# Optimization experiments

Measured on AMD Instinct MI355X. Metric: run time of the kernel, lower is better.

Reference implementation:

```python
import jax, jax.numpy as jnp
import numpy as np

B, S, DIM = 2, 2048, 2048
H, KVH, D = 16, 8, 128
EPS = 1e-6
ROPE_BASE = 1000000.0
MAX_SEQ = 8192


def _build_rope(max_seq, dim, base):
    inv_freq = 1.0 / (base ** (np.arange(0, dim, 2, dtype=np.float64) / dim))
    t = np.arange(max_seq, dtype=np.float64)
    freqs = np.outer(t, inv_freq)  # [max_seq, dim//2]
    return (jnp.asarray(np.cos(freqs), jnp.float32),
            jnp.asarray(np.sin(freqs), jnp.float32))


def setup_inputs() -> dict:
    key = jax.random.key(0)
    ks = jax.random.split(key, 7)
    scale = 0.02
    cos_cache, sin_cache = _build_rope(MAX_SEQ, D, ROPE_BASE)
    return {
        "x": jax.random.normal(ks[0], (B, S, DIM), jnp.float32),
        "wq": jax.random.normal(ks[1], (DIM, H * D), jnp.float32) * scale,
        "wk": jax.random.normal(ks[2], (DIM, KVH * D), jnp.float32) * scale,
        "wv": jax.random.normal(ks[3], (DIM, KVH * D), jnp.float32) * scale,
        "wo": jax.random.normal(ks[4], (H * D, DIM), jnp.float32) * scale,
        "q_gamma": 1.0 + 0.01 * jax.random.normal(ks[5], (D,), jnp.float32),
        "k_gamma": 1.0 + 0.01 * jax.random.normal(ks[6], (D,), jnp.float32),
        "cos_cache": cos_cache,
        "sin_cache": sin_cache,
    }


def _rmsnorm(t, gamma):
    var = jnp.mean(t * t, axis=-1, keepdims=True)
    return t * jax.lax.rsqrt(var + EPS) * gamma


def _rotate_half(t):
    t1, t2 = jnp.split(t, 2, axis=-1)
    return jnp.concatenate((-t2, t1), axis=-1)


def _apply_rope(t, cos, sin):
    # t: [B, S, heads, D]; cos/sin: [S, D//2]
    cos_f = jnp.concatenate((cos, cos), axis=-1)[None, :, None, :]
    sin_f = jnp.concatenate((sin, sin), axis=-1)[None, :, None, :]
    return t * cos_f + _rotate_half(t) * sin_f


def reference(x, wq, wk, wv, wo, q_gamma, k_gamma, cos_cache, sin_cache):
    b, s, _ = x.shape
    q = (x @ wq).reshape(b, s, H, D)
    k = (x @ wk).reshape(b, s, KVH, D)
    v = (x @ wv).reshape(b, s, KVH, D)
    q = _rmsnorm(q, q_gamma)
    k = _rmsnorm(k, k_gamma)
    # prefill: kv_len == q_len == s, cache empty
    cos, sin = cos_cache[:s], sin_cache[:s]
    q = _apply_rope(q, cos, sin)
    k = _apply_rope(k, cos, sin)
    # -> [B, heads, S, D]
    q = q.transpose(0, 2, 1, 3)
    k = k.transpose(0, 2, 1, 3)
    v = v.transpose(0, 2, 1, 3)
    # GQA: repeat_interleave kv heads
    g = H // KVH
    k = jnp.repeat(k, g, axis=1)
    v = jnp.repeat(v, g, axis=1)
    scale = 1.0 / jnp.sqrt(jnp.asarray(D, x.dtype))
    scores = jnp.einsum("bhqd,bhkd->bhqk", q, k) * scale
    causal = jnp.tril(jnp.ones((s, s), bool))
    scores = jnp.where(causal, scores, jnp.finfo(scores.dtype).min)
    attn = jax.nn.softmax(scores, axis=-1)
    out = jnp.einsum("bhqk,bhkd->bhqd", attn, v)
    out = out.transpose(0, 2, 1, 3).reshape(b, s, H * D)
    return out @ wo
```

## Files before the change

kernel.cpp:

```cpp
#include <hip/hip_runtime.h>
#include <hip/hip_bf16.h>


typedef __attribute__((ext_vector_type(8))) short s16x8;
typedef __attribute__((ext_vector_type(4))) float f32x4;

typedef const __attribute__((address_space(1))) void* gas_t;
typedef __attribute__((address_space(3))) void* las_t;
#define GLL16(g, l) __builtin_amdgcn_global_load_lds((gas_t)(const void*)(g), (las_t)(void*)(l), 16, 0, 0)

static __device__ __forceinline__ unsigned short f2bf(float f) {
    union { float f; unsigned u; } v; v.f = f;
    unsigned r = v.u + 0x7FFF + ((v.u >> 16) & 1);
    return (unsigned short)(r >> 16);
}
static __device__ __forceinline__ float bf2f(unsigned short h) {
    union { unsigned u; float f; } v; v.u = ((unsigned)h) << 16;
    return v.f;
}
static __device__ __forceinline__ float exp2_fast(float x) {
    float r; asm("v_exp_f32 %0, %1" : "=v"(r) : "v"(x)); return r;
}

#define SCALE_L2E 0.12751744900929f

__global__ __launch_bounds__(256) void k_convert_x(const float* __restrict__ x,
                                                   unsigned short* __restrict__ xb, int n) {
    int i = (blockIdx.x * 256 + threadIdx.x) * 8;
    if (i >= n) return;
    float4 a = *(const float4*)(x + i);
    float4 b = *(const float4*)(x + i + 4);
    s16x8 o;
    o[0] = (short)f2bf(a.x); o[1] = (short)f2bf(a.y); o[2] = (short)f2bf(a.z); o[3] = (short)f2bf(a.w);
    o[4] = (short)f2bf(b.x); o[5] = (short)f2bf(b.y); o[6] = (short)f2bf(b.z); o[7] = (short)f2bf(b.w);
    *(s16x8*)(xb + i) = o;
}

__global__ __launch_bounds__(256) void k_transpose_w(const float* __restrict__ src,
                                                     unsigned short* __restrict__ dst,
                                                     int K, int N, int nbase, int dstld) {
    __shared__ float t[32][33];
    int k0 = blockIdx.x * 32, n0 = blockIdx.y * 32;
    int tx = threadIdx.x & 31, ty0 = threadIdx.x >> 5;
    for (int p = 0; p < 4; p++) {
        int ty = ty0 + p * 8;
        t[ty][tx] = src[(size_t)(k0 + ty) * N + n0 + tx];
    }
    __syncthreads();
    for (int p = 0; p < 4; p++) {
        int ty = ty0 + p * 8;
        dst[(size_t)(nbase + n0 + ty) * dstld + k0 + tx] = f2bf(t[tx][ty]);
    }
}

__global__ __launch_bounds__(256) void k_transpose_v(const unsigned short* __restrict__ V,
                                                     unsigned short* __restrict__ Vt) {
    __shared__ unsigned short t[32][33];
    int s0 = blockIdx.x * 32, d0 = blockIdx.y * 32;
    size_t base = (size_t)blockIdx.z * 2048 * 128;
    int tx = threadIdx.x & 31, ty0 = threadIdx.x >> 5;
    for (int p = 0; p < 4; p++) {
        int ty = ty0 + p * 8;
        t[ty][tx] = V[base + (size_t)(s0 + ty) * 128 + d0 + tx];
    }
    __syncthreads();
    for (int p = 0; p < 4; p++) {
        int ty = ty0 + p * 8;
        Vt[base + (size_t)(d0 + ty) * 2048 + s0 + tx] = t[tx][ty];
    }
}

template<int OUTF32>
__global__ __launch_bounds__(512, 2) void k_gemm256(const unsigned short* __restrict__ A,
                                                    const unsigned short* __restrict__ Bt,
                                                    void* __restrict__ Cout,
                                                    int M, int N, int K) {
    __shared__ unsigned short Ls[2][2][2][8192];
    int tid = threadIdx.x, lane = tid & 63, wave = tid >> 6;
    int wm = wave >> 2, wn = wave & 3;
    int lr = lane & 15, lg = lane >> 4;
    int swrow = wave * 16 + (lane >> 2);
    int scol  = (lane & 3) * 8;
    const unsigned short* Ab = A  + (size_t)(blockIdx.x * 256) * K;
    const unsigned short* Bb = Bt + (size_t)(blockIdx.y * 256) * K;

    f32x4 acc[8][4] = {};
    int NK = K / 64;

    auto issue = [&](int slot, int mat, int kk, int k0) {
        const unsigned short* base = mat ? Bb : Ab;
        unsigned short* dst = &Ls[slot][mat][kk][wave * 512];
        GLL16(base + (size_t)swrow * K + k0 + kk * 32 + scol, dst);
        GLL16(base + (size_t)(swrow + 128) * K + k0 + kk * 32 + scol, dst + 4096);
    };

    issue(0, 0, 0, 0);
    issue(0, 1, 0, 0);
    issue(0, 0, 1, 0);
    issue(0, 1, 1, 0);

    for (int t = 0; t < NK; ++t) {
        int slot = t & 1, nslot = slot ^ 1;
        int kn = (t + 1) * 64;
        bool more = (t + 1) < NK;
        const unsigned short* As0 = Ls[slot][0][0];
        const unsigned short* Bs0 = Ls[slot][1][0];
        const unsigned short* As1 = Ls[slot][0][1];
        const unsigned short* Bs1 = Ls[slot][1][1];
        s16x8 af[4], bfr[4];

        asm volatile("s_waitcnt vmcnt(4)" ::: "memory");
        __builtin_amdgcn_s_barrier();
        asm volatile("" ::: "memory");

        #pragma unroll
        for (int m = 0; m < 4; m++) af[m]  = *(const s16x8*)&As0[(wm * 128 + m * 16 + lr) * 32 + lg * 8];
        #pragma unroll
        for (int n = 0; n < 4; n++) bfr[n] = *(const s16x8*)&Bs0[(wn * 64 + n * 16 + lr) * 32 + lg * 8];
        if (more) issue(nslot, 0, 0, kn);
        __builtin_amdgcn_s_setprio(1);
        #pragma unroll
        for (int m = 0; m < 4; m++)
            #pragma unroll
            for (int n = 0; n < 4; n++)
                acc[m][n] = __builtin_amdgcn_mfma_f32_16x16x32_bf16(af[m], bfr[n], acc[m][n], 0, 0, 0);
        __builtin_amdgcn_s_setprio(0);

        #pragma unroll
        for (int m = 0; m < 4; m++) af[m] = *(const s16x8*)&As0[(wm * 128 + (m + 4) * 16 + lr) * 32 + lg * 8];
        if (more) issue(nslot, 1, 0, kn);
        __builtin_amdgcn_s_setprio(1);
        #pragma unroll
        for (int m = 0; m < 4; m++)
            #pragma unroll
            for (int n = 0; n < 4; n++)
                acc[m + 4][n] = __builtin_amdgcn_mfma_f32_16x16x32_bf16(af[m], bfr[n], acc[m + 4][n], 0, 0, 0);
        __builtin_amdgcn_s_setprio(0);

        if (more) asm volatile("s_waitcnt vmcnt(4)" ::: "memory");
        else      asm volatile("s_waitcnt vmcnt(0)" ::: "memory");
        __builtin_amdgcn_s_barrier();
        asm volatile("" ::: "memory");

        #pragma unroll
        for (int m = 0; m < 4; m++) af[m]  = *(const s16x8*)&As1[(wm * 128 + m * 16 + lr) * 32 + lg * 8];
        #pragma unroll
        for (int n = 0; n < 4; n++) bfr[n] = *(const s16x8*)&Bs1[(wn * 64 + n * 16 + lr) * 32 + lg * 8];
        if (more) issue(nslot, 0, 1, kn);
        __builtin_amdgcn_s_setprio(1);
        #pragma unroll
        for (int m = 0; m < 4; m++)
            #pragma unroll
            for (int n = 0; n < 4; n++)
                acc[m][n] = __builtin_amdgcn_mfma_f32_16x16x32_bf16(af[m], bfr[n], acc[m][n], 0, 0, 0);
        __builtin_amdgcn_s_setprio(0);

        #pragma unroll
        for (int m = 0; m < 4; m++) af[m] = *(const s16x8*)&As1[(wm * 128 + (m + 4) * 16 + lr) * 32 + lg * 8];
        if (more) issue(nslot, 1, 1, kn);
        __builtin_amdgcn_s_setprio(1);
        #pragma unroll
        for (int m = 0; m < 4; m++)
            #pragma unroll
            for (int n = 0; n < 4; n++)
                acc[m + 4][n] = __builtin_amdgcn_mfma_f32_16x16x32_bf16(af[m], bfr[n], acc[m + 4][n], 0, 0, 0);
        __builtin_amdgcn_s_setprio(0);
    }

    int rbase = blockIdx.x * 256 + wm * 128;
    int cbase = blockIdx.y * 256 + wn * 64;
    #pragma unroll
    for (int am = 0; am < 8; am++)
        #pragma unroll
        for (int n = 0; n < 4; n++)
            #pragma unroll
            for (int r = 0; r < 4; r++) {
                int row = rbase + am * 16 + lg * 4 + r;
                int col = cbase + n * 16 + lr;
                float v = acc[am][n][r];
                if (OUTF32) ((float*)Cout)[(size_t)row * N + col] = v;
                else        ((unsigned short*)Cout)[(size_t)row * N + col] = f2bf(v);
            }
}

template<int OUTF32>
__global__ __launch_bounds__(256) void k_gemm_bt(const unsigned short* __restrict__ A,
                                                 const unsigned short* __restrict__ Bt,
                                                 void* __restrict__ Cout,
                                                 int M, int N, int K) {
    __shared__ unsigned short As[128 * 32];
    __shared__ unsigned short Bs[128 * 32];
    int tid = threadIdx.x;
    int lane = tid & 63;
    int wave = tid >> 6;
    int wm = wave >> 1, wn = wave & 1;
    int lr = lane & 15, lk = (lane >> 4) * 8;
    int srow = wave * 32 + (lane >> 2);
    int scol = (lane & 3) * 8;
    const unsigned short* Ag0 = A  + (size_t)(blockIdx.x * 128 + srow) * K + scol;
    const unsigned short* Ag1 = Ag0 + (size_t)16 * K;
    const unsigned short* Bg0 = Bt + (size_t)(blockIdx.y * 128 + srow) * K + scol;
    const unsigned short* Bg1 = Bg0 + (size_t)16 * K;
    unsigned short* Asw = &As[wave * 1024];
    unsigned short* Bsw = &Bs[wave * 1024];
    f32x4 acc[4][4] = {};
    for (int k0 = 0; k0 < K; k0 += 32) {
        __syncthreads();
        GLL16(Ag0 + k0, Asw);
        GLL16(Ag1 + k0, Asw + 512);
        GLL16(Bg0 + k0, Bsw);
        GLL16(Bg1 + k0, Bsw + 512);
        __syncthreads();
        s16x8 af[4], bfr[4];
        #pragma unroll
        for (int m = 0; m < 4; m++) af[m]  = *(const s16x8*)&As[(wm * 64 + m * 16 + lr) * 32 + lk];
        #pragma unroll
        for (int n = 0; n < 4; n++) bfr[n] = *(const s16x8*)&Bs[(wn * 64 + n * 16 + lr) * 32 + lk];
        #pragma unroll
        for (int m = 0; m < 4; m++)
            #pragma unroll
            for (int n = 0; n < 4; n++)
                acc[m][n] = __builtin_amdgcn_mfma_f32_16x16x32_bf16(af[m], bfr[n], acc[m][n], 0, 0, 0);
    }
    int rbase = blockIdx.x * 128 + wm * 64;
    int cbase = blockIdx.y * 128 + wn * 64;
    #pragma unroll
    for (int m = 0; m < 4; m++)
        #pragma unroll
        for (int n = 0; n < 4; n++)
            #pragma unroll
            for (int r = 0; r < 4; r++) {
                int row = rbase + m * 16 + (lane >> 4) * 4 + r;
                int col = cbase + n * 16 + lr;
                float v = acc[m][n][r];
                if (OUTF32) ((float*)Cout)[(size_t)row * N + col] = v;
                else        ((unsigned short*)Cout)[(size_t)row * N + col] = f2bf(v);
            }
}

__global__ __launch_bounds__(256) void k_rms_rope(const unsigned short* __restrict__ qkv,
                                                  const float* __restrict__ qg,
                                                  const float* __restrict__ kg,
                                                  const float* __restrict__ cosc,
                                                  const float* __restrict__ sinc,
                                                  unsigned short* __restrict__ Qt,
                                                  unsigned short* __restrict__ Kt,
                                                  unsigned short* __restrict__ Vt) {
    int r = blockIdx.x;
    int b = r >> 11;
    int s = r & 2047;
    int tid = threadIdx.x;
    int wave = tid >> 6, lane = tid & 63;
    int sl = lane >> 4;
    int li = lane & 15;
    int d0 = li * 8;
    const unsigned short* row = qkv + (size_t)r * 4096;
    #pragma unroll
    for (int p = 0; p < 2; p++) {
        int seg = p * 16 + wave * 4 + sl;
        s16x8 raw = *(const s16x8*)(row + seg * 128 + d0);
        if (seg >= 24) {
            *(s16x8*)(Vt + ((size_t)(b * 8 + (seg - 24)) * 2048 + s) * 128 + d0) = raw;
            continue;
        }
        float e[8];
        #pragma unroll
        for (int j = 0; j < 8; j++) e[j] = bf2f((unsigned short)raw[j]);
        float ssq = 0.f;
        #pragma unroll
        for (int j = 0; j < 8; j++) ssq += e[j] * e[j];
        ssq += __shfl_xor(ssq, 1, 64);
        ssq += __shfl_xor(ssq, 2, 64);
        ssq += __shfl_xor(ssq, 4, 64);
        ssq += __shfl_xor(ssq, 8, 64);
        float rn = rsqrtf(ssq * (1.0f / 128.0f) + 1e-6f);
        const float* g = (seg < 16) ? qg : kg;
        float gs = (seg < 16) ? SCALE_L2E : 1.0f;
        float4 g0 = *(const float4*)(g + d0);
        float4 g1 = *(const float4*)(g + d0 + 4);
        float t[8];
        t[0] = e[0] * rn * g0.x * gs; t[1] = e[1] * rn * g0.y * gs;
        t[2] = e[2] * rn * g0.z * gs; t[3] = e[3] * rn * g0.w * gs;
        t[4] = e[4] * rn * g1.x * gs; t[5] = e[5] * rn * g1.y * gs;
        t[6] = e[6] * rn * g1.z * gs; t[7] = e[7] * rn * g1.w * gs;
        float pr[8];
        #pragma unroll
        for (int j = 0; j < 8; j++) pr[j] = __shfl_xor(t[j], 8, 64);
        int didx = d0 & 63;
        float4 c0 = *(const float4*)(cosc + (size_t)s * 64 + didx);
        float4 c1 = *(const float4*)(cosc + (size_t)s * 64 + didx + 4);
        float4 sn0 = *(const float4*)(sinc + (size_t)s * 64 + didx);
        float4 sn1 = *(const float4*)(sinc + (size_t)s * 64 + didx + 4);
        float cv[8] = {c0.x, c0.y, c0.z, c0.w, c1.x, c1.y, c1.z, c1.w};
        float sv[8] = {sn0.x, sn0.y, sn0.z, sn0.w, sn1.x, sn1.y, sn1.z, sn1.w};
        float sgn = (li < 8) ? -1.0f : 1.0f;
        s16x8 o;
        #pragma unroll
        for (int j = 0; j < 8; j++)
            o[j] = (short)f2bf(t[j] * cv[j] + sgn * pr[j] * sv[j]);
        unsigned short* dst = (seg < 16)
            ? Qt + ((size_t)(b * 16 + seg) * 2048 + s) * 128 + d0
            : Kt + ((size_t)(b * 8 + (seg - 16)) * 2048 + s) * 128 + d0;
        *(s16x8*)dst = o;
    }
}

__global__ __launch_bounds__(512, 4) void k_attn(const unsigned short* __restrict__ Qt,
                                                 const unsigned short* __restrict__ Kt,
                                                 const unsigned short* __restrict__ Vtg,
                                                 unsigned short* __restrict__ attn) {
    __shared__ unsigned short Ks[64][136];
    __shared__ unsigned short Vs[128][72];
    __shared__ unsigned short Ps[8][16][72];
    int bid = blockIdx.x;
    int lo = bid & 255;
    int qb, bh;
    if (bid < 256) { qb = lo & 15;        bh = lo >> 4; }
    else           { qb = 15 - (lo & 15); bh = 16 + (lo >> 4); }
    int b = bh >> 4, h = bh & 15;
    int kvh = h >> 1;
    int tid = threadIdx.x;
    int lane = tid & 63, wave = tid >> 6;
    int lr = lane & 15, lg = lane >> 4;
    int q0 = qb * 128;
    const unsigned short* Qb1 = Qt + ((size_t)bh * 2048 + q0 + wave * 16) * 128;
    const unsigned short* Kbase = Kt + (size_t)(b * 8 + kvh) * 2048 * 128;
    const unsigned short* Vtb   = Vtg + (size_t)(b * 8 + kvh) * 128 * 2048;
    s16x8 aq[4];
    #pragma unroll
    for (int f = 0; f < 4; f++)
        aq[f] = *(const s16x8*)(Qb1 + (size_t)lr * 128 + f * 32 + lg * 8);
    f32x4 out[8] = {};
    float m_q = -1e30f, l_q = 0.f;
    int qglob = q0 + wave * 16 + lr;
    int qlo   = q0 + wave * 16;
    int qhi   = qlo + 15;
    int ntiles = 2 * qb + 2;
    int krow = tid >> 4, kcol = (tid & 15) * 8;
    int vrow = tid >> 3, vcol = (tid & 7) * 8;
    s16x8 kpre[2], vpre[2];
    #pragma unroll
    for (int p = 0; p < 2; p++) {
        kpre[p] = *(const s16x8*)(Kbase + (size_t)(krow + p * 32) * 128 + kcol);
        vpre[p] = *(const s16x8*)(Vtb + (size_t)(vrow + p * 64) * 2048 + vcol);
    }

    for (int t = 0; t < ntiles; t++) {
        int k0 = t * 64;
        __syncthreads();
        #pragma unroll
        for (int p = 0; p < 2; p++) {
            *(s16x8*)&Ks[krow + p * 32][kcol] = kpre[p];
            *(s16x8*)&Vs[vrow + p * 64][vcol] = vpre[p];
        }
        __syncthreads();
        if (t + 1 < ntiles) {
            int kn = k0 + 64;
            #pragma unroll
            for (int p = 0; p < 2; p++) {
                kpre[p] = *(const s16x8*)(Kbase + (size_t)(kn + krow + p * 32) * 128 + kcol);
                vpre[p] = *(const s16x8*)(Vtb + (size_t)(vrow + p * 64) * 2048 + kn + vcol);
            }
        }
        if (k0 <= qhi) {
            f32x4 st[4] = {};
            __builtin_amdgcn_s_setprio(1);
            #pragma unroll
            for (int sub = 0; sub < 4; sub++)
                #pragma unroll
                for (int f = 0; f < 4; f++) {
                    s16x8 bk = *(const s16x8*)&Ks[sub * 16 + lr][f * 32 + lg * 8];
                    st[sub] = __builtin_amdgcn_mfma_f32_16x16x32_bf16(bk, aq[f], st[sub], 0, 0, 0);
                }
            __builtin_amdgcn_s_setprio(0);
            float mx = -1e30f;
            if (k0 + 63 > qlo) {
                #pragma unroll
                for (int sub = 0; sub < 4; sub++)
                    #pragma unroll
                    for (int r = 0; r < 4; r++) {
                        int kv = k0 + sub * 16 + lg * 4 + r;
                        if (kv > qglob) st[sub][r] = -1e30f;
                        mx = fmaxf(mx, st[sub][r]);
                    }
            } else {
                #pragma unroll
                for (int sub = 0; sub < 4; sub++)
                    #pragma unroll
                    for (int r = 0; r < 4; r++) mx = fmaxf(mx, st[sub][r]);
            }
            mx = fmaxf(mx, __shfl_xor(mx, 16, 64));
            mx = fmaxf(mx, __shfl_xor(mx, 32, 64));
            bool defer = __all(mx <= m_q + 8.0f);
            float sf = 1.0f;
            if (!defer) {
                float mnew = fmaxf(m_q, mx);
                sf = exp2_fast(m_q - mnew);
                m_q = mnew;
            }
            float rs = 0.f;
            #pragma unroll
            for (int sub = 0; sub < 4; sub++)
                #pragma unroll
                for (int r = 0; r < 4; r++) {
                    float e = exp2_fast(st[sub][r] - m_q);
                    st[sub][r] = e;
                    rs += e;
                }
            rs += __shfl_xor(rs, 16, 64);
            rs += __shfl_xor(rs, 32, 64);
            l_q = defer ? (l_q + rs) : (l_q * sf + rs);
            #pragma unroll
            for (int sub = 0; sub < 4; sub++) {
                unsigned lop  = (unsigned)f2bf(st[sub][0]) | ((unsigned)f2bf(st[sub][1]) << 16);
                unsigned hip_ = (unsigned)f2bf(st[sub][2]) | ((unsigned)f2bf(st[sub][3]) << 16);
                uint2 w; w.x = lop; w.y = hip_;
                *(uint2*)&Ps[wave][lr][sub * 16 + lg * 4] = w;
            }
            if (!defer) {
                float sfr[4];
                #pragma unroll
                for (int r = 0; r < 4; r++) sfr[r] = __shfl(sf, lg * 4 + r, 64);
                #pragma unroll
                for (int blk = 0; blk < 8; blk++)
                    #pragma unroll
                    for (int r = 0; r < 4; r++) out[blk][r] *= sfr[r];
            }
            __builtin_amdgcn_s_setprio(1);
            #pragma unroll
            for (int ks = 0; ks < 2; ks++) {
                s16x8 ap = *(const s16x8*)&Ps[wave][lr][ks * 32 + lg * 8];
                #pragma unroll
                for (int blk = 0; blk < 8; blk++) {
                    s16x8 bv = *(const s16x8*)&Vs[blk * 16 + lr][ks * 32 + lg * 8];
                    out[blk] = __builtin_amdgcn_mfma_f32_16x16x32_bf16(ap, bv, out[blk], 0, 0, 0);
                }
            }
            __builtin_amdgcn_s_setprio(0);
        }
    }
    float linv = 1.0f / l_q;
    float inv[4];
    #pragma unroll
    for (int r = 0; r < 4; r++) inv[r] = __shfl(linv, lg * 4 + r, 64);
    #pragma unroll
    for (int blk = 0; blk < 8; blk++)
        #pragma unroll
        for (int r = 0; r < 4; r++) {
            int row = q0 + wave * 16 + lg * 4 + r;
            attn[((size_t)(b * 2048) + row) * 2048 + h * 128 + blk * 16 + lr] =
                f2bf(out[blk][r] * inv[r]);
        }
}

extern "C" void kernel_launch(void* const* d_in, const int* in_sizes, int n_in,
                              void* d_out, int out_size, void* d_ws, size_t ws_size,
                              hipStream_t stream) {
    const float* x    = (const float*)d_in[0];
    const float* wq   = (const float*)d_in[1];
    const float* wk   = (const float*)d_in[2];
    const float* wv   = (const float*)d_in[3];
    const float* wo   = (const float*)d_in[4];
    const float* qg   = (const float*)d_in[5];
    const float* kg   = (const float*)d_in[6];
    const float* cosc = (const float*)d_in[7];
    const float* sinc = (const float*)d_in[8];

    char* ws = (char*)d_ws;
    unsigned short* xb   = (unsigned short*)(ws);
    unsigned short* w1t  = (unsigned short*)(ws + 16777216);
    unsigned short* w2t  = (unsigned short*)(ws + 33554432);
    unsigned short* qkv  = (unsigned short*)(ws + 41943040);
    unsigned short* Qt   = (unsigned short*)(ws + 75497472);
    unsigned short* Kt   = (unsigned short*)(ws + 92274688);
    unsigned short* Vt   = (unsigned short*)(ws + 100663296);
    unsigned short* attn = (unsigned short*)(ws + 109051904);
    unsigned short* Vtg  = qkv;

    k_convert_x<<<4096, 256, 0, stream>>>(x, xb, 8388608);
    k_transpose_w<<<dim3(64, 64), 256, 0, stream>>>(wq, w1t, 2048, 2048, 0, 2048);
    k_transpose_w<<<dim3(64, 32), 256, 0, stream>>>(wk, w1t, 2048, 1024, 2048, 2048);
    k_transpose_w<<<dim3(64, 32), 256, 0, stream>>>(wv, w1t, 2048, 1024, 3072, 2048);
    k_transpose_w<<<dim3(64, 64), 256, 0, stream>>>(wo, w2t, 2048, 2048, 0, 2048);
    k_gemm256<0><<<dim3(16, 16), 512, 0, stream>>>(xb, w1t, qkv, 4096, 4096, 2048);
    k_rms_rope<<<4096, 256, 0, stream>>>(qkv, qg, kg, cosc, sinc, Qt, Kt, Vt);
    k_transpose_v<<<dim3(64, 4, 16), 256, 0, stream>>>(Vt, Vtg);
    k_attn<<<512, 512, 0, stream>>>(Qt, Kt, Vtg, attn);
    k_gemm_bt<1><<<dim3(32, 16), 256, 0, stream>>>(attn, w2t, d_out, 4096, 2048, 2048);
}
```

Baseline: 234.7 us.

## Switch attention kernel to 32x32x16 MFMA with 32-row waves and 256 threads

The attention kernel now uses 32x32x16 bf16 MFMA tiles instead of 16x16x32. Each wave owns 32 query rows, so the block shrinks to 4 waves of 256 threads covering the same 128-query tile. The change cuts per-wave LDS fragment reads relative to MFMA work, and drops one cross-lane shuffle step in the max and sum reductions. In exchange it uses more accumulator registers per thread, and halving the block size with launch bounds (256,2) may reduce latency hiding.

```diff
diff --git a/kernel.cpp b/kernel.cpp
--- a/kernel.cpp
+++ b/kernel.cpp
@@ -4,6 +4,7 @@
 
 typedef __attribute__((ext_vector_type(8))) short s16x8;
 typedef __attribute__((ext_vector_type(4))) float f32x4;
+typedef __attribute__((ext_vector_type(16))) float f32x16;
 
 typedef const __attribute__((address_space(1))) void* gas_t;
 typedef __attribute__((address_space(3))) void* las_t;
@@ -305,13 +306,13 @@
     }
 }
 
-__global__ __launch_bounds__(512, 4) void k_attn(const unsigned short* __restrict__ Qt,
+__global__ __launch_bounds__(256, 2) void k_attn(const unsigned short* __restrict__ Qt,
                                                  const unsigned short* __restrict__ Kt,
                                                  const unsigned short* __restrict__ Vtg,
                                                  unsigned short* __restrict__ attn) {
     __shared__ unsigned short Ks[64][136];
     __shared__ unsigned short Vs[128][72];
-    __shared__ unsigned short Ps[8][16][72];
+    __shared__ unsigned short Ps[4][32][72];
     int bid = blockIdx.x;
     int lo = bid & 255;
     int qb, bh;
@@ -321,75 +322,75 @@
     int kvh = h >> 1;
     int tid = threadIdx.x;
     int lane = tid & 63, wave = tid >> 6;
-    int lr = lane & 15, lg = lane >> 4;
+    int ql = lane & 31;
+    int hf = lane >> 5;
     int q0 = qb * 128;
-    const unsigned short* Qb1 = Qt + ((size_t)bh * 2048 + q0 + wave * 16) * 128;
+    const unsigned short* Qb    = Qt + ((size_t)bh * 2048 + q0 + wave * 32 + ql) * 128;
     const unsigned short* Kbase = Kt + (size_t)(b * 8 + kvh) * 2048 * 128;
     const unsigned short* Vtb   = Vtg + (size_t)(b * 8 + kvh) * 128 * 2048;
-    s16x8 aq[4];
-    #pragma unroll
-    for (int f = 0; f < 4; f++)
-        aq[f] = *(const s16x8*)(Qb1 + (size_t)lr * 128 + f * 32 + lg * 8);
-    f32x4 out[8] = {};
+    s16x8 aq[8];
+    #pragma unroll
+    for (int ds = 0; ds < 8; ds++)
+        aq[ds] = *(const s16x8*)(Qb + ds * 16 + hf * 8);
+    f32x16 out[4] = {};
     float m_q = -1e30f, l_q = 0.f;
-    int qglob = q0 + wave * 16 + lr;
-    int qlo   = q0 + wave * 16;
-    int qhi   = qlo + 15;
+    int qglob = q0 + wave * 32 + ql;
+    int qlo   = q0 + wave * 32;
+    int qhi   = qlo + 31;
     int ntiles = 2 * qb + 2;
     int krow = tid >> 4, kcol = (tid & 15) * 8;
     int vrow = tid >> 3, vcol = (tid & 7) * 8;
-    s16x8 kpre[2], vpre[2];
-    #pragma unroll
-    for (int p = 0; p < 2; p++) {
-        kpre[p] = *(const s16x8*)(Kbase + (size_t)(krow + p * 32) * 128 + kcol);
-        vpre[p] = *(const s16x8*)(Vtb + (size_t)(vrow + p * 64) * 2048 + vcol);
+    s16x8 kpre[4], vpre[4];
+    #pragma unroll
+    for (int p = 0; p < 4; p++) {
+        kpre[p] = *(const s16x8*)(Kbase + (size_t)(krow + p * 16) * 128 + kcol);
+        vpre[p] = *(const s16x8*)(Vtb + (size_t)(vrow + p * 32) * 2048 + vcol);
     }
 
     for (int t = 0; t < ntiles; t++) {
         int k0 = t * 64;
         __syncthreads();
         #pragma unroll
-        for (int p = 0; p < 2; p++) {
-            *(s16x8*)&Ks[krow + p * 32][kcol] = kpre[p];
-            *(s16x8*)&Vs[vrow + p * 64][vcol] = vpre[p];
+        for (int p = 0; p < 4; p++) {
+            *(s16x8*)&Ks[krow + p * 16][kcol] = kpre[p];
+            *(s16x8*)&Vs[vrow + p * 32][vcol] = vpre[p];
         }
         __syncthreads();
         if (t + 1 < ntiles) {
             int kn = k0 + 64;
             #pragma unroll
-            for (int p = 0; p < 2; p++) {
-                kpre[p] = *(const s16x8*)(Kbase + (size_t)(kn + krow + p * 32) * 128 + kcol);
-                vpre[p] = *(const s16x8*)(Vtb + (size_t)(vrow + p * 64) * 2048 + kn + vcol);
+            for (int p = 0; p < 4; p++) {
+                kpre[p] = *(const s16x8*)(Kbase + (size_t)(kn + krow + p * 16) * 128 + kcol);
+                vpre[p] = *(const s16x8*)(Vtb + (size_t)(vrow + p * 32) * 2048 + kn + vcol);
             }
         }
         if (k0 <= qhi) {
-            f32x4 st[4] = {};
+            f32x16 st[2] = {};
             __builtin_amdgcn_s_setprio(1);
             #pragma unroll
-            for (int sub = 0; sub < 4; sub++)
-                #pragma unroll
-                for (int f = 0; f < 4; f++) {
-                    s16x8 bk = *(const s16x8*)&Ks[sub * 16 + lr][f * 32 + lg * 8];
-                    st[sub] = __builtin_amdgcn_mfma_f32_16x16x32_bf16(bk, aq[f], st[sub], 0, 0, 0);
+            for (int sub = 0; sub < 2; sub++)
+                #pragma unroll
+                for (int ds = 0; ds < 8; ds++) {
+                    s16x8 kf = *(const s16x8*)&Ks[sub * 32 + ql][ds * 16 + hf * 8];
+                    st[sub] = __builtin_amdgcn_mfma_f32_32x32x16_bf16(kf, aq[ds], st[sub], 0, 0, 0);
                 }
             __builtin_amdgcn_s_setprio(0);
             float mx = -1e30f;
             if (k0 + 63 > qlo) {
                 #pragma unroll
-                for (int sub = 0; sub < 4; sub++)
+                for (int sub = 0; sub < 2; sub++)
                     #pragma unroll
-                    for (int r = 0; r < 4; r++) {
-                        int kv = k0 + sub * 16 + lg * 4 + r;
+                    for (int r = 0; r < 16; r++) {
+                        int kv = k0 + sub * 32 + (r & 3) + 8 * (r >> 2) + 4 * hf;
                         if (kv > qglob) st[sub][r] = -1e30f;
                         mx = fmaxf(mx, st[sub][r]);
                     }
             } else {
                 #pragma unroll
-                for (int sub = 0; sub < 4; sub++)
+                for (int sub = 0; sub < 2; sub++)
                     #pragma unroll
-                    for (int r = 0; r < 4; r++) mx = fmaxf(mx, st[sub][r]);
-            }
-            mx = fmaxf(mx, __shfl_xor(mx, 16, 64));
+                    for (int r = 0; r < 16; r++) mx = fmaxf(mx, st[sub][r]);
+            }
             mx = fmaxf(mx, __shfl_xor(mx, 32, 64));
             bool defer = __all(mx <= m_q + 8.0f);
             float sf = 1.0f;
@@ -400,56 +401,59 @@
             }
             float rs = 0.f;
             #pragma unroll
-            for (int sub = 0; sub < 4; sub++)
-                #pragma unroll
-                for (int r = 0; r < 4; r++) {
+            for (int sub = 0; sub < 2; sub++)
+                #pragma unroll
+                for (int r = 0; r < 16; r++) {
                     float e = exp2_fast(st[sub][r] - m_q);
                     st[sub][r] = e;
                     rs += e;
                 }
-            rs += __shfl_xor(rs, 16, 64);
             rs += __shfl_xor(rs, 32, 64);
             l_q = defer ? (l_q + rs) : (l_q * sf + rs);
             #pragma unroll
-            for (int sub = 0; sub < 4; sub++) {
-                unsigned lop  = (unsigned)f2bf(st[sub][0]) | ((unsigned)f2bf(st[sub][1]) << 16);
-                unsigned hip_ = (unsigned)f2bf(st[sub][2]) | ((unsigned)f2bf(st[sub][3]) << 16);
-                uint2 w; w.x = lop; w.y = hip_;
-                *(uint2*)&Ps[wave][lr][sub * 16 + lg * 4] = w;
-            }
+            for (int sub = 0; sub < 2; sub++)
+                #pragma unroll
+                for (int g = 0; g < 4; g++) {
+                    unsigned lop  = (unsigned)f2bf(st[sub][4 * g + 0]) | ((unsigned)f2bf(st[sub][4 * g + 1]) << 16);
+                    unsigned hip_ = (unsigned)f2bf(st[sub][4 * g + 2]) | ((unsigned)f2bf(st[sub][4 * g + 3]) << 16);
+                    uint2 w; w.x = lop; w.y = hip_;
+                    *(uint2*)&Ps[wave][ql][sub * 32 + g * 8 + hf * 4] = w;
+                }
             if (!defer) {
-                float sfr[4];
-                #pragma unroll
-                for (int r = 0; r < 4; r++) sfr[r] = __shfl(sf, lg * 4 + r, 64);
-                #pragma unroll
-                for (int blk = 0; blk < 8; blk++)
+                float sfr[16];
+                #pragma unroll
+                for (int r = 0; r < 16; r++)
+                    sfr[r] = __shfl(sf, (r & 3) + 8 * (r >> 2) + 4 * hf, 64);
+                #pragma unroll
+                for (int dblk = 0; dblk < 4; dblk++)
                     #pragma unroll
-                    for (int r = 0; r < 4; r++) out[blk][r] *= sfr[r];
+                    for (int r = 0; r < 16; r++) out[dblk][r] *= sfr[r];
             }
             __builtin_amdgcn_s_setprio(1);
             #pragma unroll
-            for (int ks = 0; ks < 2; ks++) {
-                s16x8 ap = *(const s16x8*)&Ps[wave][lr][ks * 32 + lg * 8];
-                #pragma unroll
-                for (int blk = 0; blk < 8; blk++) {
-                    s16x8 bv = *(const s16x8*)&Vs[blk * 16 + lr][ks * 32 + lg * 8];
-                    out[blk] = __builtin_amdgcn_mfma_f32_16x16x32_bf16(ap, bv, out[blk], 0, 0, 0);
+            for (int ks = 0; ks < 4; ks++) {
+                s16x8 pf = *(const s16x8*)&Ps[wave][ql][ks * 16 + hf * 8];
+                #pragma unroll
+                for (int dblk = 0; dblk < 4; dblk++) {
+                    s16x8 vf = *(const s16x8*)&Vs[dblk * 32 + ql][ks * 16 + hf * 8];
+                    out[dblk] = __builtin_amdgcn_mfma_f32_32x32x16_bf16(pf, vf, out[dblk], 0, 0, 0);
                 }
             }
             __builtin_amdgcn_s_setprio(0);
         }
     }
     float linv = 1.0f / l_q;
-    float inv[4];
-    #pragma unroll
-    for (int r = 0; r < 4; r++) inv[r] = __shfl(linv, lg * 4 + r, 64);
-    #pragma unroll
-    for (int blk = 0; blk < 8; blk++)
-        #pragma unroll
-        for (int r = 0; r < 4; r++) {
-            int row = q0 + wave * 16 + lg * 4 + r;
-            attn[((size_t)(b * 2048) + row) * 2048 + h * 128 + blk * 16 + lr] =
-                f2bf(out[blk][r] * inv[r]);
+    float inv[16];
+    #pragma unroll
+    for (int r = 0; r < 16; r++)
+        inv[r] = __shfl(linv, (r & 3) + 8 * (r >> 2) + 4 * hf, 64);
+    #pragma unroll
+    for (int dblk = 0; dblk < 4; dblk++)
+        #pragma unroll
+        for (int r = 0; r < 16; r++) {
+            int row = q0 + wave * 32 + (r & 3) + 8 * (r >> 2) + 4 * hf;
+            attn[((size_t)(b * 2048) + row) * 2048 + h * 128 + dblk * 32 + ql] =
+                f2bf(out[dblk][r] * inv[r]);
         }
 }
 
@@ -485,6 +489,6 @@
     k_gemm256<0><<<dim3(16, 16), 512, 0, stream>>>(xb, w1t, qkv, 4096, 4096, 2048);
     k_rms_rope<<<4096, 256, 0, stream>>>(qkv, qg, kg, cosc, sinc, Qt, Kt, Vt);
     k_transpose_v<<<dim3(64, 4, 16), 256, 0, stream>>>(Vt, Vtg);
-    k_attn<<<512, 512, 0, stream>>>(Qt, Kt, Vtg, attn);
+    k_attn<<<512, 256, 0, stream>>>(Qt, Kt, Vtg, attn);
     k_gemm_bt<1><<<dim3(32, 16), 256, 0, stream>>>(attn, w2t, d_out, 4096, 2048, 2048);
 }
```

Result: no change. 230.1 us (-1.9%).
